# Optimization experiments

Measured on AMD Instinct MI355X. Metric: run time of the kernel, lower is better.

## Reference

```python
import jax, jax.numpy as jnp
import numpy as np

DIM = 1024
N_HEADS = 16
HEAD_DIM = DIM // N_HEADS
MLP_RATIO = 4
LN_EPS = 1e-5


def _layer_norm(x, w):
    xf = x.astype(jnp.float32)
    mu = jnp.mean(xf, axis=-1, keepdims=True)
    var = jnp.var(xf, axis=-1, keepdims=True)
    y = (xf - mu) / jnp.sqrt(var + LN_EPS)
    return y * w[None, None, :]


def _apply_rope(x, cos, sin):
    # x: (b, s, h, d); cos, sin: (s, d/2)
    c = jnp.concatenate([cos, cos], axis=-1)[None, :, None, :]  # (1,s,1,d)
    s_ = jnp.concatenate([sin, sin], axis=-1)[None, :, None, :]
    x1, x2 = jnp.split(x, 2, axis=-1)
    rot = jnp.concatenate([-x2, x1], axis=-1)
    return x * c + rot * s_


def setup_inputs() -> dict:
    key = jax.random.key(0)
    ks = jax.random.split(key, 12)
    b, s = 2, 2048
    x = jax.random.normal(ks[0], (b, s, DIM), dtype=jnp.float32)
    rot_cos = jax.random.uniform(ks[1], (1, s, 1, 1, HEAD_DIM), dtype=jnp.float32)
    rot_sin = jax.random.uniform(ks[2], (1, s, 1, 1, HEAD_DIM), dtype=jnp.float32)
    w_init = 0.02
    params = {
        'ln1_w': jnp.ones((DIM,), jnp.float32),
        'w_qkv': jax.random.normal(ks[3], (3 * DIM, DIM), jnp.float32) * w_init,
        'w_out': jax.random.normal(ks[4], (DIM, DIM), jnp.float32) * w_init,
        'ln2_w': jnp.ones((DIM,), jnp.float32),
        'w_mlp1': jax.random.normal(ks[5], (MLP_RATIO * DIM, DIM), jnp.float32) * w_init,
        'b_mlp1': jnp.zeros((MLP_RATIO * DIM,), jnp.float32),
        'w_mlp2': jax.random.normal(ks[6], (DIM, MLP_RATIO * DIM), jnp.float32) * w_init,
        'b_mlp2': jnp.zeros((DIM,), jnp.float32),
    }
    return {'x': x, 'rot_cos': rot_cos, 'rot_sin': rot_sin, **params}


def reference(x, rot_cos, rot_sin, ln1_w, w_qkv, w_out, ln2_w, w_mlp1, b_mlp1, w_mlp2, b_mlp2):
    b, s, _ = x.shape
    # _split_rotary: (1,s,1,1,hd) -> (s, hd/2)
    cos = rot_cos[0, :, 0, 0, : HEAD_DIM // 2]
    sin = rot_sin[0, :, 0, 0, : HEAD_DIM // 2]

    x_skip = x
    h1 = _layer_norm(x, ln1_w)
    qkv = jnp.einsum('bsd,ed->bse', h1, w_qkv).reshape(b, s, 3, N_HEADS, HEAD_DIM)
    q, k, v = qkv[:, :, 0], qkv[:, :, 1], qkv[:, :, 2]
    q = _apply_rope(q, cos, sin)
    k = _apply_rope(k, cos, sin)

    # causal SDPA, scale = 1/sqrt(head_dim) (flex_attention default)
    scale = 1.0 / np.sqrt(HEAD_DIM)
    scores = jnp.einsum('bqhd,bkhd->bhqk', q, k) * scale
    causal = jnp.tril(jnp.ones((s, s), dtype=bool))
    scores = jnp.where(causal[None, None], scores, -jnp.inf)
    attn = jax.nn.softmax(scores, axis=-1)
    o = jnp.einsum('bhqk,bkhd->bqhd', attn, v).reshape(b, s, DIM)

    # attn out + residual (eval: dropout off, scale=1)
    x = x_skip + jnp.einsum('bsd,ed->bse', o, w_out)

    # MLP with tanh GELU + residual
    h2 = _layer_norm(x, ln2_w)
    u = jnp.einsum('bsd,ed->bse', h2, w_mlp1) + b_mlp1
    u = jax.nn.gelu(u, approximate=True)
    m = jnp.einsum('bse,de->bsd', u, w_mlp2) + b_mlp2
    return x + m
```

## Files before the change

### kernel.cpp

```cpp
#include <hip/hip_runtime.h>
#include <hip/hip_bf16.h>
#include <math.h>


#define B_ 2
#define S_ 2048
#define D_ 1024
#define H_ 16
#define DH_ 64
#define MLP_ 4096
#define ROWS_ (B_ * S_)

typedef short bf16x8 __attribute__((ext_vector_type(8)));
typedef float f32x4 __attribute__((ext_vector_type(4)));
typedef unsigned short ushort_t;
typedef ushort_t u16x4 __attribute__((ext_vector_type(4)));
typedef unsigned int u32x2 __attribute__((ext_vector_type(2)));

__device__ __forceinline__ float wave_reduce_sum(float v) {
  #pragma unroll
  for (int off = 32; off > 0; off >>= 1) v += __shfl_down(v, off, 64);
  return v;
}

__device__ __forceinline__ ushort_t f2bf(float v) {
  __hip_bfloat16 h = __float2bfloat16(v);
  return *(ushort_t*)&h;
}
__device__ __forceinline__ float bf2f(ushort_t u) {
  unsigned int v = ((unsigned int)u) << 16;
  union { unsigned int i; float f; } c; c.i = v; return c.f;
}

__device__ __forceinline__ float exp2_fast(float x) {
#if __has_builtin(__builtin_amdgcn_exp2f)
  return __builtin_amdgcn_exp2f(x);
#else
  return exp2f(x);
#endif
}
__device__ __forceinline__ float rcp_fast(float x) {
#if __has_builtin(__builtin_amdgcn_rcpf)
  return __builtin_amdgcn_rcpf(x);
#else
  return 1.0f / x;
#endif
}

__device__ __forceinline__ void async_copy16(const void* g, void* l) {
  __builtin_amdgcn_global_load_lds(
      (const __attribute__((address_space(1))) void*)g,
      (__attribute__((address_space(3))) void*)l, 16, 0, 0);
}

__global__ __launch_bounds__(256) void cast_w_kernel(
    const float* __restrict__ s0, ushort_t* __restrict__ d0, int n0,
    const float* __restrict__ s1, ushort_t* __restrict__ d1, int n1,
    const float* __restrict__ s2, ushort_t* __restrict__ d2, int n2,
    const float* __restrict__ s3, ushort_t* __restrict__ d3, int n3) {
  const float* s; ushort_t* d; int n;
  switch (blockIdx.y) {
    case 0: s = s0; d = d0; n = n0; break;
    case 1: s = s1; d = d1; n = n1; break;
    case 2: s = s2; d = d2; n = n2; break;
    default: s = s3; d = d3; n = n3; break;
  }
  const int i = (blockIdx.x * 256 + threadIdx.x) * 4;
  if (i < n) {
    const float4 v = *reinterpret_cast<const float4*>(s + i);
    u16x4 o;
    o[0] = f2bf(v.x); o[1] = f2bf(v.y); o[2] = f2bf(v.z); o[3] = f2bf(v.w);
    *reinterpret_cast<u16x4*>(d + i) = o;
  }
}

__global__ __launch_bounds__(256) void ln_kernel(
    const float* __restrict__ x, const float* __restrict__ w,
    ushort_t* __restrict__ y) {
  const int row = blockIdx.x;
  const float4 v = reinterpret_cast<const float4*>(x + (size_t)row * D_)[threadIdx.x];
  float s  = v.x + v.y + v.z + v.w;
  float ss = v.x * v.x + v.y * v.y + v.z * v.z + v.w * v.w;
  __shared__ float red[8];
  const int wave = threadIdx.x >> 6, lane = threadIdx.x & 63;
  const float ws1 = wave_reduce_sum(s);
  const float ws2 = wave_reduce_sum(ss);
  if (lane == 0) { red[wave] = ws1; red[4 + wave] = ws2; }
  __syncthreads();
  const float tot  = red[0] + red[1] + red[2] + red[3];
  const float tot2 = red[4] + red[5] + red[6] + red[7];
  const float mu  = tot * (1.0f / D_);
  const float var = tot2 * (1.0f / D_) - mu * mu;
  const float inv = rsqrtf(var + 1e-5f);
  const float4 wv = reinterpret_cast<const float4*>(w)[threadIdx.x];
  u16x4 o;
  o[0] = f2bf((v.x - mu) * inv * wv.x);
  o[1] = f2bf((v.y - mu) * inv * wv.y);
  o[2] = f2bf((v.z - mu) * inv * wv.z);
  o[3] = f2bf((v.w - mu) * inv * wv.w);
  reinterpret_cast<u16x4*>(y + (size_t)row * D_)[threadIdx.x] = o;
}

__device__ __forceinline__ float gelu_tanh(float u) {
  const float p = u + 0.044715f * u * u * u;
  const float e = exp2_fast(-2.3022078f * p);
  return u * rcp_fast(1.0f + e);
}

template <int FUSE, int OUTBF, int QKV>
__global__ __launch_bounds__(256) void gemm_bt(
    const ushort_t* __restrict__ A, const ushort_t* __restrict__ W,
    const float* __restrict__ bias, const float* __restrict__ res,
    void* __restrict__ Cv, ushort_t* __restrict__ VtOut,
    int M, int N, int K, int sm, int sn, int rects_n) {
  __shared__ ushort_t As[3][128 * 32];
  __shared__ ushort_t Bs[3][128 * 32];
  const int tid = threadIdx.x;
  const int wave = tid >> 6, lane = tid & 63;
  const int l15 = lane & 15, quad = lane >> 4;

  const int lin = blockIdx.x;
  const int xcd = lin & 7, j = lin >> 3;
  const int rm = xcd / rects_n, rn = xcd % rects_n;
  const int m0 = (rm * sm + (j % sm)) * 128;
  const int n0 = (rn * sn + (j / sm)) * 128;
  const int wm = (wave & 1) * 64, wn = (wave >> 1) * 64;

  const int srow = tid >> 2;
  const int gcol = (((tid & 3) ^ ((srow >> 1) & 3)) * 8);
  const ushort_t* Ag = A + (size_t)(m0 + srow) * K + gcol;
  const ushort_t* Wg = W + (size_t)(n0 + srow) * K + gcol;

  f32x4 acc[4][4] = {};
  const int rslot = (quad ^ ((l15 >> 1) & 3)) * 8;

  const int NI = K >> 5;
  async_copy16(Ag,               &As[0][tid * 8]);
  async_copy16(Ag + 64 * K,      &As[0][2048 + tid * 8]);
  async_copy16(Wg,               &Bs[0][tid * 8]);
  async_copy16(Wg + 64 * K,      &Bs[0][2048 + tid * 8]);
  if (NI > 1) {
    async_copy16(Ag + 32,          &As[1][tid * 8]);
    async_copy16(Ag + 64 * K + 32, &As[1][2048 + tid * 8]);
    async_copy16(Wg + 32,          &Bs[1][tid * 8]);
    async_copy16(Wg + 64 * K + 32, &Bs[1][2048 + tid * 8]);
  }

  int st = 0;
  for (int i = 0; i < NI; ++i) {
    if (i + 1 < NI) asm volatile("s_waitcnt vmcnt(4)" ::: "memory");
    else            asm volatile("s_waitcnt vmcnt(0)" ::: "memory");
    __builtin_amdgcn_s_barrier();
    __builtin_amdgcn_sched_barrier(0);
    if (i + 2 < NI) {
      const int k2 = (i + 2) << 5;
      const int nb = (st >= 1) ? st - 1 : st + 2;
      async_copy16(Ag + k2,          &As[nb][tid * 8]);
      async_copy16(Ag + 64 * K + k2, &As[nb][2048 + tid * 8]);
      async_copy16(Wg + k2,          &Bs[nb][tid * 8]);
      async_copy16(Wg + 64 * K + k2, &Bs[nb][2048 + tid * 8]);
    }
    bf16x8 af[4], bfr[4];
    #pragma unroll
    for (int ii = 0; ii < 4; ++ii) {
      af[ii]  = *(const bf16x8*)&As[st][(wm + ii * 16 + l15) * 32 + rslot];
      bfr[ii] = *(const bf16x8*)&Bs[st][(wn + ii * 16 + l15) * 32 + rslot];
    }
    #pragma unroll
    for (int ii = 0; ii < 4; ++ii)
      #pragma unroll
      for (int jj = 0; jj < 4; ++jj)
        acc[ii][jj] = __builtin_amdgcn_mfma_f32_16x16x32_bf16(af[ii], bfr[jj], acc[ii][jj], 0, 0, 0);
    st = (st == 2) ? 0 : st + 1;
  }

  #pragma unroll
  for (int i = 0; i < 4; ++i) {
    const int mb = m0 + wm + i * 16 + quad * 4;
    #pragma unroll
    for (int jj = 0; jj < 4; ++jj) {
      const int n = n0 + wn + jj * 16 + l15;
      float cv[4];
      #pragma unroll
      for (int r = 0; r < 4; ++r) {
        float c = acc[i][jj][r];
        if (FUSE & 1) c += bias[n];
        if (FUSE & 2) c = gelu_tanh(c);
        if (FUSE & 4) c += res[(size_t)(mb + r) * N + n];
        cv[r] = c;
      }
      if (QKV && ((n0 + wn) >> 10) == 2) {
        const int d  = n & 63;
        const int hh = (n >> 6) & 15;
        const int bb = mb >> 11;
        const int ss = mb & (S_ - 1);
        u16x4 pk;
        #pragma unroll
        for (int r = 0; r < 4; ++r) pk[r] = f2bf(cv[r]);
        *(u16x4*)&VtOut[((size_t)(bb * H_ + hh) * DH_ + d) * S_ + ss] = pk;
      } else {
        #pragma unroll
        for (int r = 0; r < 4; ++r) {
          if (OUTBF) ((ushort_t*)Cv)[(size_t)(mb + r) * N + n] = f2bf(cv[r]);
          else       ((float*)Cv)[(size_t)(mb + r) * N + n]   = cv[r];
        }
      }
    }
  }
}

template <int FUSE, int OUTBF>
__global__ __launch_bounds__(256) void gemm64_bt(
    const ushort_t* __restrict__ A, const ushort_t* __restrict__ W,
    const float* __restrict__ bias, const float* __restrict__ res,
    void* __restrict__ Cv, int M, int N, int K, int sm, int sn, int rects_n) {
  __shared__ ushort_t As[3][64 * 64];
  __shared__ ushort_t Bs[3][128 * 64];
  const int tid = threadIdx.x;
  const int wave = tid >> 6, lane = tid & 63;
  const int l15 = lane & 15, quad = lane >> 4;

  const int lin = blockIdx.x;
  const int xcd = lin & 7, j = lin >> 3;
  const int rm = xcd / rects_n, rn = xcd % rects_n;
  const int m0 = (rm * sm + (j % sm)) * 64;
  const int n0 = (rn * sn + (j / sm)) * 128;
  const int wn = wave * 32;

  const int srow = tid >> 3;
  const int gcol = (((tid & 7) ^ (srow & 7)) * 8);
  const ushort_t* Ag = A + (size_t)(m0 + srow) * K + gcol;
  const ushort_t* Wg = W + (size_t)(n0 + srow) * K + gcol;

  f32x4 acc[4][2] = {};

  const int NI = K >> 6;
  #pragma unroll
  for (int i = 0; i < 2; ++i)
    async_copy16(Ag + (size_t)i * 32 * K, &As[0][i * 2048 + tid * 8]);
  #pragma unroll
  for (int i = 0; i < 4; ++i)
    async_copy16(Wg + (size_t)i * 32 * K, &Bs[0][i * 2048 + tid * 8]);
  if (NI > 1) {
    #pragma unroll
    for (int i = 0; i < 2; ++i)
      async_copy16(Ag + (size_t)i * 32 * K + 64, &As[1][i * 2048 + tid * 8]);
    #pragma unroll
    for (int i = 0; i < 4; ++i)
      async_copy16(Wg + (size_t)i * 32 * K + 64, &Bs[1][i * 2048 + tid * 8]);
  }

  int st = 0;
  for (int it = 0; it < NI; ++it) {
    if (it + 1 < NI) asm volatile("s_waitcnt vmcnt(6)" ::: "memory");
    else             asm volatile("s_waitcnt vmcnt(0)" ::: "memory");
    __builtin_amdgcn_s_barrier();
    __builtin_amdgcn_sched_barrier(0);
    if (it + 2 < NI) {
      const int k2 = (it + 2) << 6;
      const int nb = (st >= 1) ? st - 1 : st + 2;
      #pragma unroll
      for (int i = 0; i < 2; ++i)
        async_copy16(Ag + (size_t)i * 32 * K + k2, &As[nb][i * 2048 + tid * 8]);
      #pragma unroll
      for (int i = 0; i < 4; ++i)
        async_copy16(Wg + (size_t)i * 32 * K + k2, &Bs[nb][i * 2048 + tid * 8]);
    }
    #pragma unroll
    for (int kk = 0; kk < 2; ++kk) {
      const int slot = (((kk * 4 + quad) ^ (l15 & 7)) * 8);
      bf16x8 af[4], bfr[2];
      #pragma unroll
      for (int i = 0; i < 4; ++i)
        af[i] = *(const bf16x8*)&As[st][(i * 16 + l15) * 64 + slot];
      #pragma unroll
      for (int jj = 0; jj < 2; ++jj)
        bfr[jj] = *(const bf16x8*)&Bs[st][(wn + jj * 16 + l15) * 64 + slot];
      #pragma unroll
      for (int i = 0; i < 4; ++i)
        #pragma unroll
        for (int jj = 0; jj < 2; ++jj)
          acc[i][jj] = __builtin_amdgcn_mfma_f32_16x16x32_bf16(af[i], bfr[jj], acc[i][jj], 0, 0, 0);
    }
    st = (st == 2) ? 0 : st + 1;
  }

  #pragma unroll
  for (int i = 0; i < 4; ++i) {
    const int mb = m0 + i * 16 + quad * 4;
    #pragma unroll
    for (int jj = 0; jj < 2; ++jj) {
      const int n = n0 + wn + jj * 16 + l15;
      #pragma unroll
      for (int r = 0; r < 4; ++r) {
        float c = acc[i][jj][r];
        if (FUSE & 1) c += bias[n];
        if (FUSE & 2) c = gelu_tanh(c);
        if (FUSE & 4) c += res[(size_t)(mb + r) * N + n];
        if (OUTBF) ((ushort_t*)Cv)[(size_t)(mb + r) * N + n] = f2bf(c);
        else       ((float*)Cv)[(size_t)(mb + r) * N + n]   = c;
      }
    }
  }
}

__global__ __launch_bounds__(256) void rope_kernel(
    const ushort_t* __restrict__ qkv, const float* __restrict__ cosb,
    const float* __restrict__ sinb, ushort_t* __restrict__ Qo,
    ushort_t* __restrict__ Ko) {
  const int bs = blockIdx.x;
  const int s  = bs & (S_ - 1);
  const int b  = bs >> 11;
  const int t  = threadIdx.x;
  const ushort_t* base = qkv + (size_t)bs * (3 * D_);
  #pragma unroll
  for (int i = 0; i < 8; ++i) {
    const int e = i * 256 + t;
    const int which = e >> 10;
    const int rem = e & 1023;
    const int h = rem >> 6;
    const int d = rem & 63;
    const float val = bf2f(base[e]);
    float out;
    if (d < 32) {
      out = val * cosb[s * 64 + d] - bf2f(base[e + 32]) * sinb[s * 64 + d];
    } else {
      out = val * cosb[s * 64 + d - 32] + bf2f(base[e - 32]) * sinb[s * 64 + d - 32];
    }
    const size_t oidx = (((size_t)(b * H_ + h)) * S_ + s) * DH_ + d;
    if (which == 0) Qo[oidx] = f2bf(out * 0.18033688736f);
    else            Ko[oidx] = f2bf(out);
  }
}

#define PPAD 72

__global__ __launch_bounds__(256) void attn_kernel(
    const ushort_t* __restrict__ Qb, const ushort_t* __restrict__ Kb,
    const ushort_t* __restrict__ Vt, ushort_t* __restrict__ O) {
  __shared__ ushort_t Ks[2][64 * 64];
  __shared__ ushort_t Vs[2][64 * 64];
  __shared__ ushort_t Plds[4][2][16 * PPAD];

  const int tid  = threadIdx.x;
  const int wave = tid >> 6;
  const int lane = tid & 63;
  const int l15 = lane & 15, quad = lane >> 4;

  const int lin = blockIdx.x;
  const int bh  = lin & 31;
  const int u   = lin >> 5;
  const int g   = (u < 8) ? (15 - u) : (u - 8);
  const int b = bh >> 4, h = bh & 15;
  const int q0 = g * 128 + wave * 32;

  const int nch_w   = (q0 >> 6) + 1;
  const int nch_max = 2 * g + 2;

  const ushort_t* Kbh = Kb + (size_t)bh * S_ * DH_;
  const ushort_t* Vbh = Vt + (size_t)bh * DH_ * S_;

  auto stage = [&](int buf, int c) {
    const int k0s = c << 6;
    #pragma unroll
    for (int i = 0; i < 2; ++i) {
      const int idx  = i * 256 + tid;
      const int row  = idx >> 3;
      const int slot = idx & 7;
      const int scol = ((slot ^ (row & 7)) * 8);
      async_copy16(Kbh + (size_t)(k0s + row) * DH_ + scol, &Ks[buf][idx * 8]);
      async_copy16(Vbh + (size_t)row * S_ + k0s + scol,    &Vs[buf][idx * 8]);
    }
  };

  bf16x8 qb[2][2];
  #pragma unroll
  for (int t = 0; t < 2; ++t) {
    const ushort_t* qptr = Qb + ((size_t)bh * S_ + q0 + t * 16 + l15) * DH_ + quad * 8;
    qb[t][0] = *(const bf16x8*)(qptr);
    qb[t][1] = *(const bf16x8*)(qptr + 32);
  }

  f32x4 o_acc[2][4] = {};
  float m_run[2] = {-1e30f, -1e30f}, l_run[2] = {0.0f, 0.0f};

  stage(0, 0);

  for (int c = 0; c < nch_max; ++c) {
    const int st = c & 1;
    __syncthreads();
    if (c + 1 < nch_max) stage(st ^ 1, c + 1);
    if (c >= nch_w) continue;
    const int k0 = c << 6;

    bf16x8 ka[4][2];
    #pragma unroll
    for (int kt = 0; kt < 4; ++kt) {
      const int row = kt * 16 + l15;
      const int bse = row * 64, rx = row & 7;
      ka[kt][0] = *(const bf16x8*)&Ks[st][bse + ((quad ^ rx) * 8)];
      ka[kt][1] = *(const bf16x8*)&Ks[st][bse + (((4 + quad) ^ rx) * 8)];
    }

    f32x4 s_t[2][4];
    __builtin_amdgcn_s_setprio(1);
    #pragma unroll
    for (int t = 0; t < 2; ++t)
      #pragma unroll
      for (int kt = 0; kt < 4; ++kt) {
        f32x4 z = {0.0f, 0.0f, 0.0f, 0.0f};
        z = __builtin_amdgcn_mfma_f32_16x16x32_bf16(ka[kt][0], qb[t][0], z, 0, 0, 0);
        z = __builtin_amdgcn_mfma_f32_16x16x32_bf16(ka[kt][1], qb[t][1], z, 0, 0, 0);
        s_t[t][kt] = z;
      }
    __builtin_amdgcn_s_setprio(0);

    if (c == nch_w - 1) {
      #pragma unroll
      for (int t = 0; t < 2; ++t) {
        const int query = q0 + t * 16 + l15;
        #pragma unroll
        for (int kt = 0; kt < 4; ++kt)
          #pragma unroll
          for (int r = 0; r < 4; ++r)
            if (k0 + kt * 16 + quad * 4 + r > query) s_t[t][kt][r] = -1e30f;
      }
    }

    #pragma unroll
    for (int t = 0; t < 2; ++t) {
      float mx = -1e30f;
      #pragma unroll
      for (int kt = 0; kt < 4; ++kt)
        #pragma unroll
        for (int r = 0; r < 4; ++r) mx = fmaxf(mx, s_t[t][kt][r]);
      mx = fmaxf(mx, __shfl_xor(mx, 16, 64));
      mx = fmaxf(mx, __shfl_xor(mx, 32, 64));
      if (!__all(mx <= m_run[t] + 8.0f)) {
        const float m_new = fmaxf(m_run[t], mx);
        const float alpha = exp2_fast(m_run[t] - m_new);
        l_run[t] *= alpha;
        #pragma unroll
        for (int mt = 0; mt < 4; ++mt)
          #pragma unroll
          for (int r = 0; r < 4; ++r) o_acc[t][mt][r] *= alpha;
        m_run[t] = m_new;
      }
      float rs = 0.0f;
      #pragma unroll
      for (int kt = 0; kt < 4; ++kt)
        #pragma unroll
        for (int r = 0; r < 4; ++r) {
          const float e = exp2_fast(s_t[t][kt][r] - m_run[t]);
          s_t[t][kt][r] = e;
          rs += e;
        }
      rs += __shfl_xor(rs, 16, 64);
      rs += __shfl_xor(rs, 32, 64);
      l_run[t] += rs;
    }

    bf16x8 va[4][2];
    #pragma unroll
    for (int mt = 0; mt < 4; ++mt) {
      const int row = mt * 16 + l15;
      const int bse = row * 64, rx = row & 7;
      va[mt][0] = *(const bf16x8*)&Vs[st][bse + ((quad ^ rx) * 8)];
      va[mt][1] = *(const bf16x8*)&Vs[st][bse + (((4 + quad) ^ rx) * 8)];
    }

    #pragma unroll
    for (int t = 0; t < 2; ++t) {
      ushort_t* Pw = &Plds[wave][t][0];
      #pragma unroll
      for (int kt = 0; kt < 4; ++kt) {
        u32x2 wpair;
        wpair[0] = (unsigned)f2bf(s_t[t][kt][0]) | ((unsigned)f2bf(s_t[t][kt][1]) << 16);
        wpair[1] = (unsigned)f2bf(s_t[t][kt][2]) | ((unsigned)f2bf(s_t[t][kt][3]) << 16);
        *(u32x2*)&Pw[l15 * PPAD + kt * 16 + quad * 4] = wpair;
      }
      asm volatile("s_waitcnt lgkmcnt(0)" ::: "memory");
      const bf16x8 pb0 = *(const bf16x8*)&Pw[l15 * PPAD + quad * 8];
      const bf16x8 pb1 = *(const bf16x8*)&Pw[l15 * PPAD + 32 + quad * 8];
      __builtin_amdgcn_s_setprio(1);
      #pragma unroll
      for (int mt = 0; mt < 4; ++mt) {
        o_acc[t][mt] = __builtin_amdgcn_mfma_f32_16x16x32_bf16(va[mt][0], pb0, o_acc[t][mt], 0, 0, 0);
        o_acc[t][mt] = __builtin_amdgcn_mfma_f32_16x16x32_bf16(va[mt][1], pb1, o_acc[t][mt], 0, 0, 0);
      }
      __builtin_amdgcn_s_setprio(0);
    }
  }

  #pragma unroll
  for (int t = 0; t < 2; ++t) {
    const float inv = 1.0f / l_run[t];
    #pragma unroll
    for (int mt = 0; mt < 4; ++mt) {
      u16x4 pk;
      #pragma unroll
      for (int r = 0; r < 4; ++r) pk[r] = f2bf(o_acc[t][mt][r] * inv);
      *(u16x4*)&O[(((size_t)b * S_ + q0 + t * 16 + l15) * H_ + h) * DH_ + mt * 16 + quad * 4] = pk;
    }
  }
}

extern "C" void kernel_launch(void* const* d_in, const int* in_sizes, int n_in,
                              void* d_out, int out_size, void* d_ws, size_t ws_size,
                              hipStream_t stream) {
  const float* x       = (const float*)d_in[0];
  const float* rot_cos = (const float*)d_in[1];
  const float* rot_sin = (const float*)d_in[2];
  const float* ln1_w   = (const float*)d_in[3];
  const float* w_qkv   = (const float*)d_in[4];
  const float* w_out   = (const float*)d_in[5];
  const float* ln2_w   = (const float*)d_in[6];
  const float* w_mlp1  = (const float*)d_in[7];
  const float* b_mlp1  = (const float*)d_in[8];
  const float* w_mlp2  = (const float*)d_in[9];
  const float* b_mlp2  = (const float*)d_in[10];
  float* out = (float*)d_out;

  char* wsb = (char*)d_ws;
  const size_t MB = 1u << 20;
  ushort_t* h1_bf  = (ushort_t*)(wsb + 0 * MB);
  ushort_t* qkv_bf = (ushort_t*)(wsb + 8 * MB);
  ushort_t* q_bf   = (ushort_t*)(wsb + 32 * MB);
  ushort_t* k_bf   = (ushort_t*)(wsb + 40 * MB);
  ushort_t* v_t    = (ushort_t*)(wsb + 48 * MB);
  ushort_t* o_bf   = (ushort_t*)(wsb + 56 * MB);
  float*    x2     = (float*)   (wsb + 64 * MB);
  ushort_t* u_bf   = (ushort_t*)(wsb + 80 * MB);
  ushort_t* wq_bf  = (ushort_t*)(wsb + 112 * MB);
  ushort_t* wo_bf  = (ushort_t*)(wsb + 118 * MB);
  ushort_t* w1_bf  = (ushort_t*)(wsb + 120 * MB);
  ushort_t* w2_bf  = (ushort_t*)(wsb + 128 * MB);
  (void)ws_size; (void)in_sizes; (void)n_in; (void)out_size;

  dim3 b256(256);

  cast_w_kernel<<<dim3(4096, 4), b256, 0, stream>>>(
      w_qkv, wq_bf, 3 * D_ * D_, w_out, wo_bf, D_ * D_,
      w_mlp1, w1_bf, MLP_ * D_, w_mlp2, w2_bf, MLP_ * D_);
  ln_kernel<<<dim3(ROWS_), b256, 0, stream>>>(x, ln1_w, h1_bf);
  gemm_bt<0, 1, 1><<<dim3(768), b256, 0, stream>>>(
      h1_bf, wq_bf, nullptr, nullptr, qkv_bf, v_t, ROWS_, 3 * D_, D_, 16, 6, 4);
  rope_kernel<<<dim3(ROWS_), b256, 0, stream>>>(qkv_bf, rot_cos, rot_sin, q_bf, k_bf);
  attn_kernel<<<dim3(512), b256, 0, stream>>>(q_bf, k_bf, v_t, o_bf);
  gemm64_bt<4, 0><<<dim3(512), b256, 0, stream>>>(
      o_bf, wo_bf, nullptr, x, x2, ROWS_, D_, D_, 16, 4, 2);
  ln_kernel<<<dim3(ROWS_), b256, 0, stream>>>(x2, ln2_w, h1_bf);
  gemm_bt<3, 1, 0><<<dim3(1024), b256, 0, stream>>>(
      h1_bf, w1_bf, b_mlp1, nullptr, u_bf, nullptr, ROWS_, MLP_, D_, 16, 8, 4);
  gemm64_bt<5, 0><<<dim3(512), b256, 0, stream>>>(
      u_bf, w2_bf, b_mlp2, x2, out, ROWS_, D_, MLP_, 16, 4, 2);
}
```

Before: 366.8 us.

## Split attention block into 8 waves of 16 queries each

The attention kernel now launches 512 threads per block with eight waves, each owning 16 query rows instead of two 16-row tiles per wave across four waves. This raises wave-level parallelism and cuts per-wave register pressure and serial work, and K/V staging needs one async copy per thread instead of two. In exchange each K/V tile loaded from LDS into registers is reused by only 16 queries per wave, so LDS read traffic per query doubles, and the larger block may limit how many blocks fit per CU.

Result: faster. 352.4 us (-3.9%).

```diff
diff --git a/kernel.cpp b/kernel.cpp
--- a/kernel.cpp
+++ b/kernel.cpp
@@ -335,12 +335,12 @@
 
 #define PPAD 72
 
-__global__ __launch_bounds__(256) void attn_kernel(
+__global__ __launch_bounds__(512) void attn_kernel(
     const ushort_t* __restrict__ Qb, const ushort_t* __restrict__ Kb,
     const ushort_t* __restrict__ Vt, ushort_t* __restrict__ O) {
   __shared__ ushort_t Ks[2][64 * 64];
   __shared__ ushort_t Vs[2][64 * 64];
-  __shared__ ushort_t Plds[4][2][16 * PPAD];
+  __shared__ ushort_t Plds[8][16 * PPAD];
 
   const int tid  = threadIdx.x;
   const int wave = tid >> 6;
@@ -352,7 +352,7 @@
   const int u   = lin >> 5;
   const int g   = (u < 8) ? (15 - u) : (u - 8);
   const int b = bh >> 4, h = bh & 15;
-  const int q0 = g * 128 + wave * 32;
+  const int q0 = g * 128 + wave * 16;
 
   const int nch_w   = (q0 >> 6) + 1;
   const int nch_max = 2 * g + 2;
@@ -362,27 +362,22 @@
 
   auto stage = [&](int buf, int c) {
     const int k0s = c << 6;
-    #pragma unroll
-    for (int i = 0; i < 2; ++i) {
-      const int idx  = i * 256 + tid;
-      const int row  = idx >> 3;
-      const int slot = idx & 7;
-      const int scol = ((slot ^ (row & 7)) * 8);
-      async_copy16(Kbh + (size_t)(k0s + row) * DH_ + scol, &Ks[buf][idx * 8]);
-      async_copy16(Vbh + (size_t)row * S_ + k0s + scol,    &Vs[buf][idx * 8]);
-    }
+    const int row  = tid >> 3;
+    const int slot = tid & 7;
+    const int scol = ((slot ^ (row & 7)) * 8);
+    async_copy16(Kbh + (size_t)(k0s + row) * DH_ + scol, &Ks[buf][tid * 8]);
+    async_copy16(Vbh + (size_t)row * S_ + k0s + scol,    &Vs[buf][tid * 8]);
   };
 
-  bf16x8 qb[2][2];
-  #pragma unroll
-  for (int t = 0; t < 2; ++t) {
-    const ushort_t* qptr = Qb + ((size_t)bh * S_ + q0 + t * 16 + l15) * DH_ + quad * 8;
-    qb[t][0] = *(const bf16x8*)(qptr);
-    qb[t][1] = *(const bf16x8*)(qptr + 32);
-  }
-
-  f32x4 o_acc[2][4] = {};
-  float m_run[2] = {-1e30f, -1e30f}, l_run[2] = {0.0f, 0.0f};
+  bf16x8 qb[2];
+  {
+    const ushort_t* qptr = Qb + ((size_t)bh * S_ + q0 + l15) * DH_ + quad * 8;
+    qb[0] = *(const bf16x8*)(qptr);
+    qb[1] = *(const bf16x8*)(qptr + 32);
+  }
+
+  f32x4 o_acc[4] = {};
+  float m_run = -1e30f, l_run = 0.0f;
 
   stage(0, 0);
 
@@ -402,62 +397,56 @@
       ka[kt][1] = *(const bf16x8*)&Ks[st][bse + (((4 + quad) ^ rx) * 8)];
     }
 
-    f32x4 s_t[2][4];
+    f32x4 s_t[4];
     __builtin_amdgcn_s_setprio(1);
     #pragma unroll
-    for (int t = 0; t < 2; ++t)
-      #pragma unroll
-      for (int kt = 0; kt < 4; ++kt) {
-        f32x4 z = {0.0f, 0.0f, 0.0f, 0.0f};
-        z = __builtin_amdgcn_mfma_f32_16x16x32_bf16(ka[kt][0], qb[t][0], z, 0, 0, 0);
-        z = __builtin_amdgcn_mfma_f32_16x16x32_bf16(ka[kt][1], qb[t][1], z, 0, 0, 0);
-        s_t[t][kt] = z;
-      }
+    for (int kt = 0; kt < 4; ++kt) {
+      f32x4 z = {0.0f, 0.0f, 0.0f, 0.0f};
+      z = __builtin_amdgcn_mfma_f32_16x16x32_bf16(ka[kt][0], qb[0], z, 0, 0, 0);
+      z = __builtin_amdgcn_mfma_f32_16x16x32_bf16(ka[kt][1], qb[1], z, 0, 0, 0);
+      s_t[kt] = z;
+    }
     __builtin_amdgcn_s_setprio(0);
 
     if (c == nch_w - 1) {
-      #pragma unroll
-      for (int t = 0; t < 2; ++t) {
-        const int query = q0 + t * 16 + l15;
-        #pragma unroll
-        for (int kt = 0; kt < 4; ++kt)
-          #pragma unroll
-          for (int r = 0; r < 4; ++r)
-            if (k0 + kt * 16 + quad * 4 + r > query) s_t[t][kt][r] = -1e30f;
-      }
-    }
-
-    #pragma unroll
-    for (int t = 0; t < 2; ++t) {
+      const int query = q0 + l15;
+      #pragma unroll
+      for (int kt = 0; kt < 4; ++kt)
+        #pragma unroll
+        for (int r = 0; r < 4; ++r)
+          if (k0 + kt * 16 + quad * 4 + r > query) s_t[kt][r] = -1e30f;
+    }
+
+    {
       float mx = -1e30f;
       #pragma unroll
       for (int kt = 0; kt < 4; ++kt)
         #pragma unroll
-        for (int r = 0; r < 4; ++r) mx = fmaxf(mx, s_t[t][kt][r]);
+        for (int r = 0; r < 4; ++r) mx = fmaxf(mx, s_t[kt][r]);
       mx = fmaxf(mx, __shfl_xor(mx, 16, 64));
       mx = fmaxf(mx, __shfl_xor(mx, 32, 64));
-      if (!__all(mx <= m_run[t] + 8.0f)) {
-        const float m_new = fmaxf(m_run[t], mx);
-        const float alpha = exp2_fast(m_run[t] - m_new);
-        l_run[t] *= alpha;
+      if (!__all(mx <= m_run + 8.0f)) {
+        const float m_new = fmaxf(m_run, mx);
+        const float alpha = exp2_fast(m_run - m_new);
+        l_run *= alpha;
         #pragma unroll
         for (int mt = 0; mt < 4; ++mt)
           #pragma unroll
-          for (int r = 0; r < 4; ++r) o_acc[t][mt][r] *= alpha;
-        m_run[t] = m_new;
+          for (int r = 0; r < 4; ++r) o_acc[mt][r] *= alpha;
+        m_run = m_new;
       }
       float rs = 0.0f;
       #pragma unroll
       for (int kt = 0; kt < 4; ++kt)
         #pragma unroll
         for (int r = 0; r < 4; ++r) {
-          const float e = exp2_fast(s_t[t][kt][r] - m_run[t]);
-          s_t[t][kt][r] = e;
+          const float e = exp2_fast(s_t[kt][r] - m_run);
+          s_t[kt][r] = e;
           rs += e;
         }
       rs += __shfl_xor(rs, 16, 64);
       rs += __shfl_xor(rs, 32, 64);
-      l_run[t] += rs;
+      l_run += rs;
     }
 
     bf16x8 va[4][2];
@@ -469,14 +458,13 @@
       va[mt][1] = *(const bf16x8*)&Vs[st][bse + (((4 + quad) ^ rx) * 8)];
     }
 
-    #pragma unroll
-    for (int t = 0; t < 2; ++t) {
-      ushort_t* Pw = &Plds[wave][t][0];
+    {
+      ushort_t* Pw = &Plds[wave][0];
       #pragma unroll
       for (int kt = 0; kt < 4; ++kt) {
         u32x2 wpair;
-        wpair[0] = (unsigned)f2bf(s_t[t][kt][0]) | ((unsigned)f2bf(s_t[t][kt][1]) << 16);
-        wpair[1] = (unsigned)f2bf(s_t[t][kt][2]) | ((unsigned)f2bf(s_t[t][kt][3]) << 16);
+        wpair[0] = (unsigned)f2bf(s_t[kt][0]) | ((unsigned)f2bf(s_t[kt][1]) << 16);
+        wpair[1] = (unsigned)f2bf(s_t[kt][2]) | ((unsigned)f2bf(s_t[kt][3]) << 16);
         *(u32x2*)&Pw[l15 * PPAD + kt * 16 + quad * 4] = wpair;
       }
       asm volatile("s_waitcnt lgkmcnt(0)" ::: "memory");
@@ -485,22 +473,21 @@
       __builtin_amdgcn_s_setprio(1);
       #pragma unroll
       for (int mt = 0; mt < 4; ++mt) {
-        o_acc[t][mt] = __builtin_amdgcn_mfma_f32_16x16x32_bf16(va[mt][0], pb0, o_acc[t][mt], 0, 0, 0);
-        o_acc[t][mt] = __builtin_amdgcn_mfma_f32_16x16x32_bf16(va[mt][1], pb1, o_acc[t][mt], 0, 0, 0);
+        o_acc[mt] = __builtin_amdgcn_mfma_f32_16x16x32_bf16(va[mt][0], pb0, o_acc[mt], 0, 0, 0);
+        o_acc[mt] = __builtin_amdgcn_mfma_f32_16x16x32_bf16(va[mt][1], pb1, o_acc[mt], 0, 0, 0);
       }
       __builtin_amdgcn_s_setprio(0);
     }
   }
 
-  #pragma unroll
-  for (int t = 0; t < 2; ++t) {
-    const float inv = 1.0f / l_run[t];
+  {
+    const float inv = 1.0f / l_run;
     #pragma unroll
     for (int mt = 0; mt < 4; ++mt) {
       u16x4 pk;
       #pragma unroll
-      for (int r = 0; r < 4; ++r) pk[r] = f2bf(o_acc[t][mt][r] * inv);
-      *(u16x4*)&O[(((size_t)b * S_ + q0 + t * 16 + l15) * H_ + h) * DH_ + mt * 16 + quad * 4] = pk;
+      for (int r = 0; r < 4; ++r) pk[r] = f2bf(o_acc[mt][r] * inv);
+      *(u16x4*)&O[(((size_t)b * S_ + q0 + l15) * H_ + h) * DH_ + mt * 16 + quad * 4] = pk;
     }
   }
 }
@@ -546,7 +533,7 @@
   gemm_bt<0, 1, 1><<<dim3(768), b256, 0, stream>>>(
       h1_bf, wq_bf, nullptr, nullptr, qkv_bf, v_t, ROWS_, 3 * D_, D_, 16, 6, 4);
   rope_kernel<<<dim3(ROWS_), b256, 0, stream>>>(qkv_bf, rot_cos, rot_sin, q_bf, k_bf);
-  attn_kernel<<<dim3(512), b256, 0, stream>>>(q_bf, k_bf, v_t, o_bf);
+  attn_kernel<<<dim3(512), dim3(512), 0, stream>>>(q_bf, k_bf, v_t, o_bf);
   gemm64_bt<4, 0><<<dim3(512), b256, 0, stream>>>(
       o_bf, wo_bf, nullptr, x, x2, ROWS_, D_, D_, 16, 4, 2);
   ln_kernel<<<dim3(ROWS_), b256, 0, stream>>>(x2, ln2_w, h1_bf);
```
